# Optimization experiments

Measured on AMD Instinct MI355X. Metric: run time of the kernel, lower is better.

## Reference

```python
import jax, jax.numpy as jnp
import numpy as np

POSE_IDS = np.array([0, 4, 8, 12, 16])
BN_EPS = 1e-5


def setup_inputs() -> dict:
    key = jax.random.key(0)
    ks = jax.random.split(key, 8)
    N, C, H, W = 64, 2048, 24, 12
    P, Cl = 5, 256
    Cm = C + P * Cl  # 3328
    return {
        "x": jax.random.normal(ks[0], (N, C, H, W), jnp.float32),
        "poses": jax.random.uniform(ks[1], (N, 17, 4), jnp.float32),
        "local_w": jax.random.normal(ks[2], (P, Cl, C), jnp.float32) * 0.02,
        "local_b": jnp.zeros((P, Cl), jnp.float32),
        "local_gamma": jnp.ones((P, Cl), jnp.float32),
        "local_beta": jnp.zeros((P, Cl), jnp.float32),
        "local_mean": jax.random.normal(ks[3], (P, Cl), jnp.float32) * 0.1,
        "local_var": jax.random.uniform(ks[4], (P, Cl), jnp.float32, 0.5, 1.5),
        "merge_w": jax.random.normal(ks[5], (C, Cm), jnp.float32) * 0.02,
        "merge_b": jnp.zeros((C,), jnp.float32),
        "merge_gamma": jnp.ones((C,), jnp.float32),
        "merge_beta": jnp.zeros((C,), jnp.float32),
        "merge_mean": jax.random.normal(ks[6], (C,), jnp.float32) * 0.1,
        "merge_var": jax.random.uniform(ks[7], (C,), jnp.float32, 0.5, 1.5),
    }


def reference(x, poses, local_w, local_b, local_gamma, local_beta, local_mean,
              local_var, merge_w, merge_b, merge_gamma, merge_beta, merge_mean,
              merge_var):
    N, C, H, W = x.shape
    kp = poses[:, jnp.asarray(POSE_IDS), :]  # [N,P,4]
    # box = [left, top, w, h]; clamp to [0, 0.75]; scale whole box by confidence
    half = jnp.full_like(kp[..., 0], 0.5)
    box = jnp.stack([kp[..., 0] - 0.25, kp[..., 1] - 0.25, half, half], axis=-1)
    box = jnp.clip(box, 0.0, 0.75) * kp[..., 2:3]
    # integer ROI bounds on the feature grid (round-half-to-even like torch)
    xs = jnp.maximum(0, jnp.round(W * box[..., 0])).astype(jnp.int32)          # [N,P]
    xe = jnp.minimum(W - 1, jnp.round(W * (box[..., 0] + box[..., 2]))).astype(jnp.int32)
    ys = jnp.maximum(0, jnp.round(H * box[..., 1])).astype(jnp.int32)
    ye = jnp.minimum(H - 1, jnp.round(H * (box[..., 1] + box[..., 3]))).astype(jnp.int32)
    rows = jnp.arange(H)
    cols = jnp.arange(W)
    mh = (rows[None, None, :] >= ys[..., None]) & (rows[None, None, :] < ye[..., None])  # [N,P,H]
    mw = (cols[None, None, :] >= xs[..., None]) & (cols[None, None, :] < xe[..., None])  # [N,P,W]
    mask = (mh[..., :, None] & mw[..., None, :]).astype(x.dtype)  # [N,P,H,W]
    # masked average pool over the ROI (single pass over x)
    sums = jnp.einsum('nchw,nphw->npc', x, mask)
    area = ((ye - ys) * (xe - xs)).astype(x.dtype)
    avg = sums / jnp.where(area > 0, area, 1.0)[..., None]  # [N,P,C], 0 for empty ROIs
    # per-part 1x1 conv + BN(eval) + ReLU -> [N,P,Cl]
    loc = jnp.einsum('npc,pkc->npk', avg, local_w) + local_b[None]
    loc = (loc - local_mean[None]) * (local_gamma[None] / jnp.sqrt(local_var[None] + BN_EPS)) + local_beta[None]
    loc = jax.nn.relu(loc)
    # global max pool -> [N,C]
    gfeat = x.max(axis=(2, 3))
    cat = jnp.concatenate([loc.reshape(N, -1), gfeat], axis=1)  # [N, P*Cl + C]
    # merge 1x1 conv + BN(eval) + ReLU
    y = cat @ merge_w.T + merge_b
    y = (y - merge_mean) * (merge_gamma / jnp.sqrt(merge_var + BN_EPS)) + merge_beta
    y = jax.nn.relu(y)
    # F.normalize(p=2, dim=1)
    norm = jnp.linalg.norm(y, axis=1, keepdims=True)
    return y / jnp.maximum(norm, 1e-12)
```

## Files before the change

### kernel.cpp

```cpp
#include <hip/hip_runtime.h>

#define N_   64
#define C_   2048
#define HW_  288
#define P_   5
#define CM_  3328
#define LOC_ 1280
#define SEGC 8
#define SEGM 13

template<int CTRL, int RMASK>
__device__ __forceinline__ float dpp_term(float x) {
  return __int_as_float(__builtin_amdgcn_update_dpp(0, __float_as_int(x), CTRL, RMASK, 0xF, true));
}
__device__ __forceinline__ float wave_sum63(float x) {
  x += dpp_term<0xB1, 0xF>(x);
  x += dpp_term<0x4E, 0xF>(x);
  x += dpp_term<0x141,0xF>(x);
  x += dpp_term<0x140,0xF>(x);
  x += dpp_term<0x142,0xA>(x);
  x += dpp_term<0x143,0xC>(x);
  return x;
}
__device__ __forceinline__ float wave_max63(float x) {
  x = fmaxf(x, dpp_term<0xB1, 0xF>(x));
  x = fmaxf(x, dpp_term<0x4E, 0xF>(x));
  x = fmaxf(x, dpp_term<0x141,0xF>(x));
  x = fmaxf(x, dpp_term<0x140,0xF>(x));
  x = fmaxf(x, dpp_term<0x142,0xA>(x));
  x = fmaxf(x, dpp_term<0x143,0xC>(x));
  return x;
}

__global__ __launch_bounds__(256) void kA(const float* __restrict__ poses,
    const float* __restrict__ lb, const float* __restrict__ lg, const float* __restrict__ lbe,
    const float* __restrict__ lm, const float* __restrict__ lv,
    const float* __restrict__ mb, const float* __restrict__ mg, const float* __restrict__ mbe,
    const float* __restrict__ mm, const float* __restrict__ mv,
    unsigned* __restrict__ mh, unsigned* __restrict__ mw, float* __restrict__ inva,
    float* __restrict__ locA, float* __restrict__ locB,
    float* __restrict__ mrgA, float* __restrict__ mrgB) {
  int t = blockIdx.x * 256 + threadIdx.x;
  if (t < 320) {
    int n = t / 5, p = t - 5 * (t / 5);
    const float* kp = poses + ((size_t)n * 17 + 4 * p) * 4;
    float px = kp[0], py = kp[1], z = kp[2];
    float bx = fminf(fmaxf(px - 0.25f, 0.f), 0.75f) * z;
    float by = fminf(fmaxf(py - 0.25f, 0.f), 0.75f) * z;
    float bw = 0.5f * z;
    float bh = 0.5f * z;
    int xs = (int)fmaxf(0.f,  rintf(12.f * bx));
    int xe = (int)fminf(11.f, rintf(12.f * (bx + bw)));
    int ys = (int)fmaxf(0.f,  rintf(24.f * by));
    int ye = (int)fminf(23.f, rintf(24.f * (by + bh)));
    mh[t] = ((1u << ye) - 1u) & ~((1u << ys) - 1u);
    mw[t] = ((1u << xe) - 1u) & ~((1u << xs) - 1u);
    int area = (ye - ys) * (xe - xs);
    inva[t] = area > 0 ? 1.f / (float)area : 1.f;
  } else if (t < 320 + LOC_) {
    int i = t - 320;
    float sc = lg[i] / sqrtf(lv[i] + 1e-5f);
    locA[i] = sc;
    locB[i] = (lb[i] - lm[i]) * sc + lbe[i];
  } else if (t < 320 + LOC_ + C_) {
    int j = t - 320 - LOC_;
    float sc = mg[j] / sqrtf(mv[j] + 1e-5f);
    mrgA[j] = sc;
    mrgB[j] = (mb[j] - mm[j]) * sc + mbe[j];
  }
}

__global__ __launch_bounds__(256) void kB(const float* __restrict__ x,
    const unsigned* __restrict__ mhv, const unsigned* __restrict__ mwv,
    const float* __restrict__ inva,
    float* __restrict__ avg, float* __restrict__ cat) {
  int gw   = (blockIdx.x << 2) | (threadIdx.x >> 6);
  int lane = threadIdx.x & 63;
  int n = gw >> 11;
  int c = gw & 2047;
  const float4* xp = (const float4*)(x + (size_t)gw * HW_);
  unsigned MH[P_], MW[P_];
#pragma unroll
  for (int p = 0; p < P_; ++p) { MH[p] = mhv[n * P_ + p]; MW[p] = mwv[n * P_ + p]; }
  float s[P_] = {0.f, 0.f, 0.f, 0.f, 0.f};
  float4 v = xp[lane];
  int e0 = lane << 2;
  int h  = e0 / 12;
  int w0 = e0 - h * 12;
  float mx = fmaxf(fmaxf(v.x, v.y), fmaxf(v.z, v.w));
#pragma unroll
  for (int p = 0; p < P_; ++p) {
    unsigned bits = (0u - ((MH[p] >> h) & 1u)) & (MW[p] >> w0);
    s[p] += (bits & 1u) ? v.x : 0.f;
    s[p] += (bits & 2u) ? v.y : 0.f;
    s[p] += (bits & 4u) ? v.z : 0.f;
    s[p] += (bits & 8u) ? v.w : 0.f;
  }
  if (lane < 8) {
    float4 v2 = xp[64 + lane];
    int e1 = 256 + (lane << 2);
    int h1 = e1 / 12;
    int w1 = e1 - h1 * 12;
    mx = fmaxf(mx, fmaxf(fmaxf(v2.x, v2.y), fmaxf(v2.z, v2.w)));
#pragma unroll
    for (int p = 0; p < P_; ++p) {
      unsigned bits = (0u - ((MH[p] >> h1) & 1u)) & (MW[p] >> w1);
      s[p] += (bits & 1u) ? v2.x : 0.f;
      s[p] += (bits & 2u) ? v2.y : 0.f;
      s[p] += (bits & 4u) ? v2.z : 0.f;
      s[p] += (bits & 8u) ? v2.w : 0.f;
    }
  }
  mx = wave_max63(mx);
#pragma unroll
  for (int p = 0; p < P_; ++p) s[p] = wave_sum63(s[p]);
  if (lane == 63) {
    cat[(size_t)n * CM_ + LOC_ + c] = mx;
#pragma unroll
    for (int p = 0; p < P_; ++p)
      avg[((size_t)n * P_ + p) * C_ + c] = s[p] * inva[n * P_ + p];
  }
}

template<int GSEG>
__device__ __forceinline__ void gemm_tile(const float* __restrict__ Ag, int lda,
                                          const float* __restrict__ Wg, int ldw,
                                          float* __restrict__ Og, int ldo,
                                          float* As, float* Ws) {
  const int t  = threadIdx.x;
  const int nq = t & 15;
  const int kq = t >> 4;
  const int c4 = (t & 15) << 2;
  const int rr = t >> 4;
  float acc[4][4] = {};
  for (int g = 0; g < GSEG; ++g) {
    __syncthreads();
#pragma unroll
    for (int i = 0; i < 4; ++i) {
      int r = rr + (i << 4);
      *(float4*)&As[r * 68 + c4] = *(const float4*)&Ag[(size_t)r * lda + (g << 6) + c4];
      *(float4*)&Ws[r * 68 + c4] = *(const float4*)&Wg[(size_t)r * ldw + (g << 6) + c4];
    }
    __syncthreads();
#pragma unroll
    for (int c = 0; c < 64; c += 4) {
      float4 a[4], w[4];
#pragma unroll
      for (int i = 0; i < 4; ++i) a[i] = *(const float4*)&As[(nq + (i << 4)) * 68 + c];
#pragma unroll
      for (int j = 0; j < 4; ++j) w[j] = *(const float4*)&Ws[(kq + (j << 4)) * 68 + c];
#pragma unroll
      for (int i = 0; i < 4; ++i)
#pragma unroll
        for (int j = 0; j < 4; ++j)
          acc[i][j] += a[i].x * w[j].x + a[i].y * w[j].y + a[i].z * w[j].z + a[i].w * w[j].w;
    }
  }
#pragma unroll
  for (int i = 0; i < 4; ++i)
#pragma unroll
    for (int j = 0; j < 4; ++j)
      Og[(size_t)(nq + (i << 4)) * ldo + kq + (j << 4)] = acc[i][j];
}

__global__ __launch_bounds__(256) void kC(const float* __restrict__ avg,
                                          const float* __restrict__ local_w,
                                          float* __restrict__ locP) {
  __shared__ float As[64 * 68];
  __shared__ float Ws[64 * 68];
  int b  = blockIdx.x;
  int tl = b >> 3;
  int sg = b & 7;
  int p  = tl >> 2;
  int kt = tl & 3;
  const float* Ag = avg + p * C_ + (sg << 8);
  const float* Wg = local_w + ((size_t)p * 256 + (kt << 6)) * C_ + (sg << 8);
  float* Og = locP + (size_t)sg * (N_ * LOC_) + (p << 8) + (kt << 6);
  gemm_tile<4>(Ag, P_ * C_, Wg, C_, Og, LOC_, As, Ws);
}

__global__ __launch_bounds__(256) void kC2(const float* __restrict__ locP,
                                           const float* __restrict__ locA,
                                           const float* __restrict__ locB,
                                           float* __restrict__ cat) {
  int i = blockIdx.x * 256 + threadIdx.x;
  int n = i / LOC_;
  int q = i - n * LOC_;
  float s = 0.f;
#pragma unroll
  for (int sg = 0; sg < SEGC; ++sg) s += locP[(size_t)sg * (N_ * LOC_) + i];
  float v = s * locA[q] + locB[q];
  cat[(size_t)n * CM_ + q] = fmaxf(v, 0.f);
}

__global__ __launch_bounds__(256) void kD(const float* __restrict__ cat,
                                          const float* __restrict__ merge_w,
                                          float* __restrict__ mrgP) {
  __shared__ float As[64 * 68];
  __shared__ float Ws[64 * 68];
  int b  = blockIdx.x;
  int jt = b / SEGM;
  int sg = b - jt * SEGM;
  const float* Ag = cat + (sg << 8);
  const float* Wg = merge_w + (size_t)(jt << 6) * CM_ + (sg << 8);
  float* Og = mrgP + (size_t)sg * (N_ * C_) + (jt << 6);
  gemm_tile<4>(Ag, CM_, Wg, CM_, Og, C_, As, Ws);
}

__global__ __launch_bounds__(256) void kE(const float* __restrict__ mrgP,
                                          const float* __restrict__ mrgA,
                                          const float* __restrict__ mrgB,
                                          float* __restrict__ out) {
  int n = blockIdx.x, t = threadIdx.x;
  float z[8]; float ss = 0.f;
#pragma unroll
  for (int r = 0; r < 8; ++r) {
    int j = t + (r << 8);
    float y = 0.f;
#pragma unroll
    for (int sg = 0; sg < SEGM; ++sg) y += mrgP[(size_t)sg * (N_ * C_) + (size_t)n * C_ + j];
    float v = y * mrgA[j] + mrgB[j];
    v = fmaxf(v, 0.f);
    z[r] = v; ss += v * v;
  }
#pragma unroll
  for (int off = 32; off; off >>= 1) ss += __shfl_xor(ss, off, 64);
  __shared__ float red[4];
  if ((t & 63) == 0) red[t >> 6] = ss;
  __syncthreads();
  float tot = red[0] + red[1] + red[2] + red[3];
  float inv = 1.f / fmaxf(sqrtf(tot), 1e-12f);
#pragma unroll
  for (int r = 0; r < 8; ++r) out[(size_t)n * C_ + t + (r << 8)] = z[r] * inv;
}

extern "C" void kernel_launch(void* const* d_in, const int* in_sizes, int n_in,
                              void* d_out, int out_size, void* d_ws, size_t ws_size,
                              hipStream_t stream) {
  const float* x          = (const float*)d_in[0];
  const float* poses      = (const float*)d_in[1];
  const float* local_w    = (const float*)d_in[2];
  const float* local_b    = (const float*)d_in[3];
  const float* local_g    = (const float*)d_in[4];
  const float* local_be   = (const float*)d_in[5];
  const float* local_m    = (const float*)d_in[6];
  const float* local_v    = (const float*)d_in[7];
  const float* merge_w    = (const float*)d_in[8];
  const float* merge_b    = (const float*)d_in[9];
  const float* merge_g    = (const float*)d_in[10];
  const float* merge_be   = (const float*)d_in[11];
  const float* merge_m    = (const float*)d_in[12];
  const float* merge_v    = (const float*)d_in[13];

  float* ws   = (float*)d_ws;
  float* cat  = ws;
  float* avg  = ws + 212992;
  float* locP = ws + 868352;
  float* mrgP = ws + 1523712;
  float* prm  = ws + 3227648;
  unsigned* mh = (unsigned*)(prm);
  unsigned* mw = (unsigned*)(prm + 320);
  float* inva = prm + 640;
  float* locA = prm + 960;
  float* locB = prm + 2240;
  float* mrgA = prm + 3520;
  float* mrgB = prm + 5568;

  kA<<<15, 256, 0, stream>>>(poses, local_b, local_g, local_be, local_m, local_v,
                             merge_b, merge_g, merge_be, merge_m, merge_v,
                             mh, mw, inva, locA, locB, mrgA, mrgB);
  kB<<<(N_ * C_) / 4, 256, 0, stream>>>(x, mh, mw, inva, avg, cat);
  kC<<<20 * SEGC, 256, 0, stream>>>(avg, local_w, locP);
  kC2<<<(N_ * LOC_) / 256, 256, 0, stream>>>(locP, locA, locB, cat);
  kD<<<32 * SEGM, 256, 0, stream>>>(cat, merge_w, mrgP);
  kE<<<N_, 256, 0, stream>>>(mrgP, mrgA, mrgB, (float*)d_out);
}
```

Measured before the change: 315.7 us.

## Fold parameter-prep kernel into consumers and prefetch GEMM tiles into registers

Removes the separate kA launch: ROI masks and inverse areas are now computed per wave inside kB straight from poses, and the BN scale and shift are computed inline in kC2 and kE. The shared GEMM tile routine now register-prefetches the next K-slice while computing on the current one. This saves one launch plus a small global round trip, and hides global load latency in the GEMMs. In exchange, the pose and box math is repeated by every wave, and the prefetch raises register pressure.

```diff
diff --git a/kernel.cpp b/kernel.cpp
--- a/kernel.cpp
+++ b/kernel.cpp
@@ -32,18 +32,19 @@
   return x;
 }
 
-__global__ __launch_bounds__(256) void kA(const float* __restrict__ poses,
-    const float* __restrict__ lb, const float* __restrict__ lg, const float* __restrict__ lbe,
-    const float* __restrict__ lm, const float* __restrict__ lv,
-    const float* __restrict__ mb, const float* __restrict__ mg, const float* __restrict__ mbe,
-    const float* __restrict__ mm, const float* __restrict__ mv,
-    unsigned* __restrict__ mh, unsigned* __restrict__ mw, float* __restrict__ inva,
-    float* __restrict__ locA, float* __restrict__ locB,
-    float* __restrict__ mrgA, float* __restrict__ mrgB) {
-  int t = blockIdx.x * 256 + threadIdx.x;
-  if (t < 320) {
-    int n = t / 5, p = t - 5 * (t / 5);
-    const float* kp = poses + ((size_t)n * 17 + 4 * p) * 4;
+__global__ __launch_bounds__(256) void kB(const float* __restrict__ x,
+    const float* __restrict__ poses,
+    float* __restrict__ avg, float* __restrict__ cat) {
+  int gw   = (blockIdx.x << 2) | (threadIdx.x >> 6);
+  int lane = threadIdx.x & 63;
+  int n = gw >> 11;
+  int c = gw & 2047;
+  unsigned MH[P_], MW[P_];
+  float INV[P_];
+  const float* kpn = poses + (size_t)n * 68;
+#pragma unroll
+  for (int p = 0; p < P_; ++p) {
+    const float* kp = kpn + 16 * p;
     float px = kp[0], py = kp[1], z = kp[2];
     float bx = fminf(fmaxf(px - 0.25f, 0.f), 0.75f) * z;
     float by = fminf(fmaxf(py - 0.25f, 0.f), 0.75f) * z;
@@ -53,35 +54,12 @@
     int xe = (int)fminf(11.f, rintf(12.f * (bx + bw)));
     int ys = (int)fmaxf(0.f,  rintf(24.f * by));
     int ye = (int)fminf(23.f, rintf(24.f * (by + bh)));
-    mh[t] = ((1u << ye) - 1u) & ~((1u << ys) - 1u);
-    mw[t] = ((1u << xe) - 1u) & ~((1u << xs) - 1u);
+    MH[p] = ((1u << ye) - 1u) & ~((1u << ys) - 1u);
+    MW[p] = ((1u << xe) - 1u) & ~((1u << xs) - 1u);
     int area = (ye - ys) * (xe - xs);
-    inva[t] = area > 0 ? 1.f / (float)area : 1.f;
-  } else if (t < 320 + LOC_) {
-    int i = t - 320;
-    float sc = lg[i] / sqrtf(lv[i] + 1e-5f);
-    locA[i] = sc;
-    locB[i] = (lb[i] - lm[i]) * sc + lbe[i];
-  } else if (t < 320 + LOC_ + C_) {
-    int j = t - 320 - LOC_;
-    float sc = mg[j] / sqrtf(mv[j] + 1e-5f);
-    mrgA[j] = sc;
-    mrgB[j] = (mb[j] - mm[j]) * sc + mbe[j];
-  }
-}
-
-__global__ __launch_bounds__(256) void kB(const float* __restrict__ x,
-    const unsigned* __restrict__ mhv, const unsigned* __restrict__ mwv,
-    const float* __restrict__ inva,
-    float* __restrict__ avg, float* __restrict__ cat) {
-  int gw   = (blockIdx.x << 2) | (threadIdx.x >> 6);
-  int lane = threadIdx.x & 63;
-  int n = gw >> 11;
-  int c = gw & 2047;
+    INV[p] = area > 0 ? 1.f / (float)area : 1.f;
+  }
   const float4* xp = (const float4*)(x + (size_t)gw * HW_);
-  unsigned MH[P_], MW[P_];
-#pragma unroll
-  for (int p = 0; p < P_; ++p) { MH[p] = mhv[n * P_ + p]; MW[p] = mwv[n * P_ + p]; }
   float s[P_] = {0.f, 0.f, 0.f, 0.f, 0.f};
   float4 v = xp[lane];
   int e0 = lane << 2;
@@ -118,7 +96,7 @@
     cat[(size_t)n * CM_ + LOC_ + c] = mx;
 #pragma unroll
     for (int p = 0; p < P_; ++p)
-      avg[((size_t)n * P_ + p) * C_ + c] = s[p] * inva[n * P_ + p];
+      avg[((size_t)n * P_ + p) * C_ + c] = s[p] * INV[p];
   }
 }
 
@@ -132,16 +110,31 @@
   const int kq = t >> 4;
   const int c4 = (t & 15) << 2;
   const int rr = t >> 4;
+  float4 pA[4], pW[4];
+#pragma unroll
+  for (int i = 0; i < 4; ++i) {
+    int r = rr + (i << 4);
+    pA[i] = *(const float4*)&Ag[(size_t)r * lda + c4];
+    pW[i] = *(const float4*)&Wg[(size_t)r * ldw + c4];
+  }
   float acc[4][4] = {};
   for (int g = 0; g < GSEG; ++g) {
     __syncthreads();
 #pragma unroll
     for (int i = 0; i < 4; ++i) {
       int r = rr + (i << 4);
-      *(float4*)&As[r * 68 + c4] = *(const float4*)&Ag[(size_t)r * lda + (g << 6) + c4];
-      *(float4*)&Ws[r * 68 + c4] = *(const float4*)&Wg[(size_t)r * ldw + (g << 6) + c4];
+      *(float4*)&As[r * 68 + c4] = pA[i];
+      *(float4*)&Ws[r * 68 + c4] = pW[i];
     }
     __syncthreads();
+    if (g + 1 < GSEG) {
+#pragma unroll
+      for (int i = 0; i < 4; ++i) {
+        int r = rr + (i << 4);
+        pA[i] = *(const float4*)&Ag[(size_t)r * lda + ((g + 1) << 6) + c4];
+        pW[i] = *(const float4*)&Wg[(size_t)r * ldw + ((g + 1) << 6) + c4];
+      }
+    }
 #pragma unroll
     for (int c = 0; c < 64; c += 4) {
       float4 a[4], w[4];
@@ -180,16 +173,17 @@
 }
 
 __global__ __launch_bounds__(256) void kC2(const float* __restrict__ locP,
-                                           const float* __restrict__ locA,
-                                           const float* __restrict__ locB,
-                                           float* __restrict__ cat) {
+    const float* __restrict__ lb, const float* __restrict__ lg, const float* __restrict__ lbe,
+    const float* __restrict__ lm, const float* __restrict__ lv,
+    float* __restrict__ cat) {
   int i = blockIdx.x * 256 + threadIdx.x;
   int n = i / LOC_;
   int q = i - n * LOC_;
   float s = 0.f;
 #pragma unroll
   for (int sg = 0; sg < SEGC; ++sg) s += locP[(size_t)sg * (N_ * LOC_) + i];
-  float v = s * locA[q] + locB[q];
+  float sc = lg[q] / sqrtf(lv[q] + 1e-5f);
+  float v = (s + lb[q] - lm[q]) * sc + lbe[q];
   cat[(size_t)n * CM_ + q] = fmaxf(v, 0.f);
 }
 
@@ -208,9 +202,9 @@
 }
 
 __global__ __launch_bounds__(256) void kE(const float* __restrict__ mrgP,
-                                          const float* __restrict__ mrgA,
-                                          const float* __restrict__ mrgB,
-                                          float* __restrict__ out) {
+    const float* __restrict__ mb, const float* __restrict__ mg, const float* __restrict__ mbe,
+    const float* __restrict__ mm, const float* __restrict__ mv,
+    float* __restrict__ out) {
   int n = blockIdx.x, t = threadIdx.x;
   float z[8]; float ss = 0.f;
 #pragma unroll
@@ -219,7 +213,8 @@
     float y = 0.f;
 #pragma unroll
     for (int sg = 0; sg < SEGM; ++sg) y += mrgP[(size_t)sg * (N_ * C_) + (size_t)n * C_ + j];
-    float v = y * mrgA[j] + mrgB[j];
+    float sc = mg[j] / sqrtf(mv[j] + 1e-5f);
+    float v = (y + mb[j] - mm[j]) * sc + mbe[j];
     v = fmaxf(v, 0.f);
     z[r] = v; ss += v * v;
   }
@@ -257,21 +252,12 @@
   float* avg  = ws + 212992;
   float* locP = ws + 868352;
   float* mrgP = ws + 1523712;
-  float* prm  = ws + 3227648;
-  unsigned* mh = (unsigned*)(prm);
-  unsigned* mw = (unsigned*)(prm + 320);
-  float* inva = prm + 640;
-  float* locA = prm + 960;
-  float* locB = prm + 2240;
-  float* mrgA = prm + 3520;
-  float* mrgB = prm + 5568;
-
-  kA<<<15, 256, 0, stream>>>(poses, local_b, local_g, local_be, local_m, local_v,
-                             merge_b, merge_g, merge_be, merge_m, merge_v,
-                             mh, mw, inva, locA, locB, mrgA, mrgB);
-  kB<<<(N_ * C_) / 4, 256, 0, stream>>>(x, mh, mw, inva, avg, cat);
+
+  kB<<<(N_ * C_) / 4, 256, 0, stream>>>(x, poses, avg, cat);
   kC<<<20 * SEGC, 256, 0, stream>>>(avg, local_w, locP);
-  kC2<<<(N_ * LOC_) / 256, 256, 0, stream>>>(locP, locA, locB, cat);
+  kC2<<<(N_ * LOC_) / 256, 256, 0, stream>>>(locP, local_b, local_g, local_be,
+                                             local_m, local_v, cat);
   kD<<<32 * SEGM, 256, 0, stream>>>(cat, merge_w, mrgP);
-  kE<<<N_, 256, 0, stream>>>(mrgP, mrgA, mrgB, (float*)d_out);
-}
+  kE<<<N_, 256, 0, stream>>>(mrgP, merge_b, merge_g, merge_be, merge_m, merge_v,
+                             (float*)d_out);
+}
```

Measured after the change: 374.7 us. 18.7% more time.
